# Kernel optimization log

Measured on AMD Instinct MI355X. Metric: run time of the kernel, lower is better.

The kernel has to match this reference:

```python
import jax, jax.numpy as jnp
import numpy as np

B, T, D, H = 1, 2048, 1024, 16
Dh = D // H
GSA_SCALE = 0.25
LN_EPS = 1e-5


def setup_inputs() -> dict:
    key = jax.random.key(0)
    ks = jax.random.split(key, 24)
    s = 0.02
    def W(k, din, dout):
        return jax.random.normal(k, (din, dout), jnp.float32) * s
    inp = dict(
        x=jax.random.normal(ks[0], (B, T, D), jnp.float32),
        mask=jnp.ones((B, T, T), jnp.bool_),
        # MultiHeadAttention params (linears[0..3] = q,k,v,o)
        mha_wq=W(ks[1], D, D), mha_bq=jnp.zeros((D,), jnp.float32),
        mha_wk=W(ks[2], D, D), mha_bk=jnp.zeros((D,), jnp.float32),
        mha_wv=W(ks[3], D, D), mha_bv=jnp.zeros((D,), jnp.float32),
        mha_wo=W(ks[4], D, D), mha_bo=jnp.zeros((D,), jnp.float32),
        # _GeodesicSelfAttention params
        gsa_wq=W(ks[5], D, D), gsa_bq=jnp.zeros((D,), jnp.float32),
        gsa_wk=W(ks[6], D, D), gsa_bk=jnp.zeros((D,), jnp.float32),
        gsa_wv=W(ks[7], D, D), gsa_bv=jnp.zeros((D,), jnp.float32),
        gsa_wo=W(ks[8], D, D), gsa_bo=jnp.zeros((D,), jnp.float32),
        log_diag=jnp.zeros((H, Dh), jnp.float32),  # nn.Parameter(torch.zeros(h, dk))
        # LayerNorms
        ln_mha_g=jnp.ones((D,), jnp.float32), ln_mha_b=jnp.zeros((D,), jnp.float32),
        ln_gsa_g=jnp.ones((D,), jnp.float32), ln_gsa_b=jnp.zeros((D,), jnp.float32),
        # mix scalar (initialized to -2.0 in __init__)
        gsa_mix=jnp.asarray(-2.0, jnp.float32),
        # gate: Linear(D,D) -> GELU -> Linear(D,1), last bias filled with 0.5
        gate_w1=W(ks[9], D, D), gate_b1=jnp.zeros((D,), jnp.float32),
        gate_w2=W(ks[10], D, 1), gate_b2=jnp.full((1,), 0.5, jnp.float32),
    )
    return inp


def _ln(x, g, b):
    m = x.mean(-1, keepdims=True)
    v = ((x - m) ** 2).mean(-1, keepdims=True)
    return (x - m) / jnp.sqrt(v + LN_EPS) * g + b


def _heads(y):  # [B,T,D] -> [B,H,T,Dh]
    return y.reshape(B, T, H, Dh).transpose(0, 2, 1, 3)


def _merge(y):  # [B,H,T,Dh] -> [B,T,D]
    return y.transpose(0, 2, 1, 3).reshape(B, T, D)


def _forward(x, mask, mha_wq, mha_bq, mha_wk, mha_bk, mha_wv, mha_bv, mha_wo, mha_bo,
             gsa_wq, gsa_bq, gsa_wk, gsa_bk, gsa_wv, gsa_bv, gsa_wo, gsa_bo,
             log_diag, ln_mha_g, ln_mha_b, ln_gsa_g, ln_gsa_b, gsa_mix,
             gate_w1, gate_b1, gate_w2, gate_b2):
    inv_sqrt_dh = 1.0 / jnp.sqrt(jnp.float32(Dh))
    m4 = mask[:, None, :, :]  # [B,1,T,T]

    # ---- standard MHA branch ----
    q = _heads(x @ mha_wq + mha_bq)
    k = _heads(x @ mha_wk + mha_bk)
    v = _heads(x @ mha_wv + mha_bv)
    scores = jnp.einsum('bhtd,bhsd->bhts', q, k) * inv_sqrt_dh
    scores = jnp.where(m4, scores, -jnp.inf)
    p = jax.nn.softmax(scores, axis=-1)
    mha_out = _merge(jnp.einsum('bhts,bhsd->bhtd', p, v)) @ mha_wo + mha_bo

    # ---- geodesic (Mahalanobis) branch ----
    qg = _heads(x @ gsa_wq + gsa_bq)
    kg = _heads(x @ gsa_wk + gsa_bk)
    vg = _heads(x @ gsa_wv + gsa_bv)
    diag = jax.nn.softplus(log_diag) + 1e-6          # [H,Dh]
    diag4 = diag[None, :, None, :]
    qM = qg * diag4
    q2M = (qg * qM).sum(-1)                           # [B,H,T]
    k2M = (kg * (kg * diag4)).sum(-1)                 # [B,H,T]
    cross = jnp.einsum('bhtd,bhsd->bhts', qM, kg)     # [B,H,T,T]
    dist = q2M[..., :, None] + k2M[..., None, :] - 2.0 * cross
    s = -0.5 * dist * inv_sqrt_dh
    s = jnp.where(m4, s, -jnp.inf)
    all_inf = jnp.all(jnp.isneginf(s), axis=-1, keepdims=True)
    s = jnp.where(all_inf, 0.0, s)
    pg = jax.nn.softmax(s * GSA_SCALE, axis=-1)
    gsa_out = _merge(jnp.einsum('bhts,bhsd->bhtd', pg, vg)) @ gsa_wo + gsa_bo

    # ---- gated mix ----
    mha_out = _ln(mha_out, ln_mha_g, ln_mha_b)
    gsa_out = jax.nn.sigmoid(gsa_mix) * _ln(gsa_out, ln_gsa_g, ln_gsa_b)
    g = jax.nn.gelu(x @ gate_w1 + gate_b1, approximate=False) @ gate_w2 + gate_b2
    alpha = 0.9 * jax.nn.sigmoid(g)                   # alpha_cap = 0.9, [B,T,1]
    return alpha * mha_out + (1.0 - alpha) * gsa_out


def reference(x, mask, mha_wq, mha_bq, mha_wk, mha_bk, mha_wv, mha_bv, mha_wo, mha_bo,
              gsa_wq, gsa_bq, gsa_wk, gsa_bk, gsa_wv, gsa_bv, gsa_wo, gsa_bo,
              log_diag, ln_mha_g, ln_mha_b, ln_gsa_g, ln_gsa_b, gsa_mix,
              gate_w1, gate_b1, gate_w2, gate_b2):
    return _forward(x, mask, mha_wq, mha_bq, mha_wk, mha_bk, mha_wv, mha_bv, mha_wo, mha_bo,
                    gsa_wq, gsa_bq, gsa_wk, gsa_bk, gsa_wv, gsa_bv, gsa_wo, gsa_bo,
                    log_diag, ln_mha_g, ln_mha_b, ln_gsa_g, ln_gsa_b, gsa_mix,
                    gate_w1, gate_b1, gate_w2, gate_b2)
```

## Files before the change

kernel.cpp:

```cpp
#include <hip/hip_runtime.h>
#include <stdint.h>

typedef unsigned short u16;
typedef u16   u16x4  __attribute__((ext_vector_type(4)));
typedef u16   u16x8  __attribute__((ext_vector_type(8)));
typedef __bf16 bf16x8 __attribute__((ext_vector_type(8)));
typedef float f32x4  __attribute__((ext_vector_type(4)));

#define SEQ   2048
#define DM    1024
#define NHEAD 16
#define DHEAD 64

#define QM_SCALE 0.180336880f
#define QG_SCALE 0.045084220f
#define K2_SCALE 0.022542110f

static __device__ __forceinline__ u16 f2b(float f) {
  uint32_t u = __float_as_uint(f);
  u += 0x7fffu + ((u >> 16) & 1u);
  return (u16)(u >> 16);
}
static __device__ __forceinline__ float b2f(u16 u) {
  return __uint_as_float(((uint32_t)u) << 16);
}

static __device__ __forceinline__ void gload16(const u16* g, u16* l) {
  __builtin_amdgcn_global_load_lds(
      (const __attribute__((address_space(1))) unsigned int*)g,
      (__attribute__((address_space(3))) unsigned int*)l, 16, 0, 0);
}

struct PrepArgs { const float* w[9]; u16* o[9];
                  const float* x; u16* xb; const float* log_diag; float* diag; };

__global__ __launch_bounds__(256) void prep_kernel(PrepArgs a) {
  const int z = blockIdx.z, tid = threadIdx.x;
  if (z == 9) {
    int b = blockIdx.y * 16 + blockIdx.x;
#pragma unroll
    for (int j = 0; j < 8; ++j) {
      int idx = b * 8192 + j * 1024 + tid * 4;
      float4 v = *(const float4*)&a.x[idx];
      u16x4 w = {f2b(v.x), f2b(v.y), f2b(v.z), f2b(v.w)};
      *(u16x4*)&a.xb[idx] = w;
    }
    if (b == 0) {
#pragma unroll
      for (int j = 0; j < 4; ++j) {
        int i = j * 256 + tid;
        float v = a.log_diag[i];
        float sp = (v > 20.f) ? v : log1pf(__expf(v));
        a.diag[i] = sp + 1e-6f;
      }
    }
    return;
  }
  const float* __restrict__ src = a.w[z];
  u16* __restrict__ dst = a.o[z];
  int r0 = blockIdx.y * 64, c0 = blockIdx.x * 64;
  __shared__ float tile[64][65];
  int r = tid >> 2, o8 = (tid & 3) * 16;
#pragma unroll
  for (int i = 0; i < 16; i += 4) {
    float4 v = *(const float4*)&src[(r0 + r) * DM + c0 + o8 + i];
    tile[r][o8 + i + 0] = v.x; tile[r][o8 + i + 1] = v.y;
    tile[r][o8 + i + 2] = v.z; tile[r][o8 + i + 3] = v.w;
  }
  __syncthreads();
  u16x8 w0, w1;
#pragma unroll
  for (int i = 0; i < 8; ++i) w0[i] = f2b(tile[o8 + i][r]);
#pragma unroll
  for (int i = 0; i < 8; ++i) w1[i] = f2b(tile[o8 + 8 + i][r]);
  *(u16x8*)&dst[(c0 + r) * DM + r0 + o8]     = w0;
  *(u16x8*)&dst[(c0 + r) * DM + r0 + o8 + 8] = w1;
}

struct GemmDesc { const u16* A; const u16* Bt; const float* bias; void* out;
                  float* aux; int mode; int k0; int klen; float scale; };
struct GemmParams { GemmDesc d[8]; const float* diag; };

__global__ __launch_bounds__(256) void gemm_bt_kernel(GemmParams p) {
  GemmDesc g = p.d[blockIdx.z];
  const int K = DM;
  const int m0 = blockIdx.y * 128, n0 = blockIdx.x * 64;
  const int tid = threadIdx.x;
  const int wave = tid >> 6, lane = tid & 63, ln = lane & 15, quad = lane >> 4;

  __shared__ __align__(16) u16 As[2 * 128 * 32];
  __shared__ __align__(16) u16 Bs[2 * 64 * 32];

  const f32x4 fz = {0.f, 0.f, 0.f, 0.f};
  f32x4 acc[2][4];
#pragma unroll
  for (int i = 0; i < 2; ++i)
#pragma unroll
    for (int j = 0; j < 4; ++j) acc[i][j] = fz;

  const u16* Aps[4]; const u16* Bps[2];
#pragma unroll
  for (int s = 0; s < 4; ++s) {
    int vr = s * 64 + (tid >> 2);
    Aps[s] = g.A + (size_t)(m0 + (vr & 127)) * K + g.k0 + (vr >> 7) * 32 + (tid & 3) * 8;
  }
#pragma unroll
  for (int s = 0; s < 2; ++s) {
    int vr = s * 64 + (tid >> 2);
    Bps[s] = g.Bt + (size_t)(n0 + (vr & 63)) * K + g.k0 + (vr >> 6) * 32 + (tid & 3) * 8;
  }

  for (int kk = 0; kk < g.klen; kk += 64) {
#pragma unroll
    for (int s = 0; s < 4; ++s) gload16(Aps[s] + kk, &As[s * 2048 + tid * 8]);
#pragma unroll
    for (int s = 0; s < 2; ++s) gload16(Bps[s] + kk, &Bs[s * 2048 + tid * 8]);
    __syncthreads();
#pragma unroll
    for (int c = 0; c < 2; ++c) {
      bf16x8 af[2], bfr[4];
#pragma unroll
      for (int mb = 0; mb < 2; ++mb)
        af[mb] = *(const bf16x8*)&As[(c * 128 + wave * 32 + mb * 16 + ln) * 32 + quad * 8];
#pragma unroll
      for (int nb = 0; nb < 4; ++nb)
        bfr[nb] = *(const bf16x8*)&Bs[(c * 64 + nb * 16 + ln) * 32 + quad * 8];
#pragma unroll
      for (int mb = 0; mb < 2; ++mb)
#pragma unroll
        for (int nb = 0; nb < 4; ++nb)
          acc[mb][nb] = __builtin_amdgcn_mfma_f32_16x16x32_bf16(af[mb], bfr[nb], acc[mb][nb], 0, 0, 0);
    }
    __syncthreads();
  }

  const int mode = g.mode;
  const int h = n0 >> 6;
#pragma unroll
  for (int mb = 0; mb < 2; ++mb) {
    int row = m0 + wave * 32 + mb * 16 + quad * 4;
    float ksum[4] = {0.f, 0.f, 0.f, 0.f};
#pragma unroll
    for (int nb = 0; nb < 4; ++nb) {
      int col = n0 + nb * 16 + ln;
      float bv = g.bias ? g.bias[col] : 0.f;
      f32x4 a = acc[mb][nb];
      if (mode == 5) {
        u16x4 w;
#pragma unroll
        for (int r = 0; r < 4; ++r) w[r] = f2b(a[r] + bv);
        *(u16x4*)&((u16*)g.out)[((size_t)(h * 64) + nb * 16 + ln) * SEQ + row] = w;
        continue;
      }
#pragma unroll
      for (int r = 0; r < 4; ++r) {
        float v = a[r] + bv;
        int rw = row + r;
        if (mode == 0) {
          ((u16*)g.out)[((size_t)h * SEQ + rw) * DHEAD + (col & 63)] = f2b(v);
        } else if (mode == 1) {
          ((u16*)g.out)[((size_t)h * SEQ + rw) * DHEAD + (col & 63)] = f2b(v * g.scale);
        } else if (mode == 2) {
          ((u16*)g.out)[((size_t)h * SEQ + rw) * DHEAD + (col & 63)] = f2b(v * p.diag[col] * g.scale);
        } else if (mode == 3) {
          float gg = 0.5f * v * (1.f + erff(v * 0.70710678f));
          ((u16*)g.out)[(size_t)rw * DM + col] = f2b(gg);
        } else if (mode == 4) {
          ((float*)g.out)[(size_t)rw * DM + col] = v;
        } else {
          ((u16*)g.out)[((size_t)h * SEQ + rw) * DHEAD + (col & 63)] = f2b(v);
          ksum[r] += v * v * p.diag[col];
        }
      }
    }
    if (mode == 6) {
#pragma unroll
      for (int r = 0; r < 4; ++r) {
        float s = ksum[r];
        s += __shfl_xor(s, 1); s += __shfl_xor(s, 2);
        s += __shfl_xor(s, 4); s += __shfl_xor(s, 8);
        if (ln == 0) g.aux[(size_t)h * SEQ + row + r] = s * K2_SCALE;
      }
    }
  }
}

__global__ __launch_bounds__(256) void flash_kernel(
    const u16* __restrict__ Qm, const u16* __restrict__ Km, const u16* __restrict__ VmT,
    const u16* __restrict__ Qg, const u16* __restrict__ Kg, const u16* __restrict__ VgT,
    const float* __restrict__ k2m, u16* __restrict__ attM, u16* __restrict__ attG) {
  const int z = blockIdx.z;
  const u16* __restrict__ Q  = z ? Qg  : Qm;
  const u16* __restrict__ Kp = z ? Kg  : Km;
  const u16* __restrict__ Vt = z ? VgT : VmT;
  u16* __restrict__ out = z ? attG : attM;
  const int h = blockIdx.y;
  const int tid = threadIdx.x, wave = tid >> 6, lane = tid & 63, ln = lane & 15, quad = lane >> 4;
  const int wrow = blockIdx.x * 128 + wave * 32;

  __shared__ __align__(16) u16 Ks[64 * 72];
  __shared__ __align__(16) u16 Vs[80 * 72];
  __shared__ __align__(16) u16 Pt[4][32 * 72];
  __shared__ float k2s[64];

  bf16x8 qf[2][2];
#pragma unroll
  for (int qb = 0; qb < 2; ++qb)
#pragma unroll
    for (int kb = 0; kb < 2; ++kb)
      qf[qb][kb] = *(const bf16x8*)&Q[((size_t)(h * SEQ) + wrow + qb * 16 + ln) * 64 + kb * 32 + quad * 8];

  const f32x4 fz = {0.f, 0.f, 0.f, 0.f};
  f32x4 o[2][5];
#pragma unroll
  for (int qb = 0; qb < 2; ++qb)
#pragma unroll
    for (int db = 0; db < 5; ++db) o[qb][db] = fz;

  const int sr = tid >> 2, sc = (tid & 3) * 16;
  const u16* Kbase = Kp + (size_t)h * SEQ * 64;
  const u16* Vbase = Vt + (size_t)h * 64 * SEQ;

  if (tid < 36) ((uint32_t*)&Vs[64 * 72])[tid] = 0x3F803F80u;

  u16x8 kr0 = *(const u16x8*)&Kbase[(size_t)sr * 64 + sc];
  u16x8 kr1 = *(const u16x8*)&Kbase[(size_t)sr * 64 + sc + 8];
  u16x8 vr0 = *(const u16x8*)&Vbase[(size_t)sr * SEQ + sc];
  u16x8 vr1 = *(const u16x8*)&Vbase[(size_t)sr * SEQ + sc + 8];
  float k2r = 0.f;
  if (z && tid < 64) k2r = k2m[h * SEQ + tid];

  for (int kt = 0; kt < SEQ; kt += 64) {
    *(u16x8*)&Ks[sr * 72 + sc]     = kr0;
    *(u16x8*)&Ks[sr * 72 + sc + 8] = kr1;
    *(u16x8*)&Vs[sr * 72 + sc]     = vr0;
    *(u16x8*)&Vs[sr * 72 + sc + 8] = vr1;
    if (z && tid < 64) k2s[tid] = k2r;
    __syncthreads();
    if (kt + 64 < SEQ) {
      kr0 = *(const u16x8*)&Kbase[(size_t)(kt + 64 + sr) * 64 + sc];
      kr1 = *(const u16x8*)&Kbase[(size_t)(kt + 64 + sr) * 64 + sc + 8];
      vr0 = *(const u16x8*)&Vbase[(size_t)sr * SEQ + kt + 64 + sc];
      vr1 = *(const u16x8*)&Vbase[(size_t)sr * SEQ + kt + 64 + sc + 8];
      if (z && tid < 64) k2r = k2m[h * SEQ + kt + 64 + tid];
    }

    bf16x8 kf0[4], kf1[4];
#pragma unroll
    for (int sb = 0; sb < 4; ++sb) {
      kf0[sb] = *(const bf16x8*)&Ks[(sb * 16 + ln) * 72 + quad * 8];
      kf1[sb] = *(const bf16x8*)&Ks[(sb * 16 + ln) * 72 + 32 + quad * 8];
    }

#pragma unroll
    for (int qb = 0; qb < 2; ++qb) {
      f32x4 st[4];
#pragma unroll
      for (int sb = 0; sb < 4; ++sb) {
        st[sb] = fz;
        st[sb] = __builtin_amdgcn_mfma_f32_16x16x32_bf16(kf0[sb], qf[qb][0], st[sb], 0, 0, 0);
        st[sb] = __builtin_amdgcn_mfma_f32_16x16x32_bf16(kf1[sb], qf[qb][1], st[sb], 0, 0, 0);
      }
#pragma unroll
      for (int sb = 0; sb < 4; ++sb) {
        if (z) {
          f32x4 b4 = *(const f32x4*)&k2s[sb * 16 + quad * 4];
#pragma unroll
          for (int r = 0; r < 4; ++r) st[sb][r] -= b4[r];
        }
        uint32_t eb[4];
#pragma unroll
        for (int r = 0; r < 4; ++r)
          eb[r] = __float_as_uint(__builtin_amdgcn_exp2f(st[sb][r]));
        uint32_t lo = __builtin_amdgcn_perm(eb[1], eb[0], 0x07060302u);
        uint32_t hi = __builtin_amdgcn_perm(eb[3], eb[2], 0x07060302u);
        uint2 pk = {lo, hi};
        *(uint2*)&Pt[wave][(qb * 16 + ln) * 72 + sb * 16 + quad * 4] = pk;
      }
    }
    __asm__ __volatile__("" ::: "memory");

    bf16x8 pf[2][2];
#pragma unroll
    for (int qb = 0; qb < 2; ++qb) {
      pf[qb][0] = *(const bf16x8*)&Pt[wave][(qb * 16 + ln) * 72 + quad * 8];
      pf[qb][1] = *(const bf16x8*)&Pt[wave][(qb * 16 + ln) * 72 + 32 + quad * 8];
    }
#pragma unroll
    for (int db = 0; db < 5; ++db) {
      bf16x8 vf0 = *(const bf16x8*)&Vs[(db * 16 + ln) * 72 + quad * 8];
      bf16x8 vf1 = *(const bf16x8*)&Vs[(db * 16 + ln) * 72 + 32 + quad * 8];
#pragma unroll
      for (int qb = 0; qb < 2; ++qb) {
        o[qb][db] = __builtin_amdgcn_mfma_f32_16x16x32_bf16(vf0, pf[qb][0], o[qb][db], 0, 0, 0);
        o[qb][db] = __builtin_amdgcn_mfma_f32_16x16x32_bf16(vf1, pf[qb][1], o[qb][db], 0, 0, 0);
      }
    }
    __syncthreads();
  }

#pragma unroll
  for (int qb = 0; qb < 2; ++qb) {
    float l_all = __shfl(o[qb][4][0], ln);
    float inv = 1.f / l_all;
#pragma unroll
    for (int db = 0; db < 4; ++db) {
      u16x4 w;
#pragma unroll
      for (int r = 0; r < 4; ++r) w[r] = f2b(o[qb][db][r] * inv);
      *(u16x4*)&out[(size_t)(wrow + qb * 16 + ln) * DM + h * 64 + db * 16 + quad * 4] = w;
    }
  }
}

__global__ __launch_bounds__(256) void final_kernel(
    const float* __restrict__ p0, const float* __restrict__ p1,
    const float* __restrict__ p2, const float* __restrict__ p3,
    const u16* __restrict__ G1, const float* __restrict__ w2,
    const float* __restrict__ b2, const float* __restrict__ mixp,
    const float* __restrict__ gm, const float* __restrict__ bm,
    const float* __restrict__ gg, const float* __restrict__ bg,
    float* __restrict__ out) {
  int t = blockIdx.x, tid = threadIdx.x;
  float xm[4], xg[4];
  float sm = 0.f, sm2 = 0.f, sg = 0.f, sg2 = 0.f, sd = 0.f;
#pragma unroll
  for (int j0 = 0; j0 < 4; ++j0) {
    int j = tid + j0 * 256;
    size_t idx = (size_t)t * DM + j;
    float a = p0[idx] + p1[idx];
    float b = p2[idx] + p3[idx];
    xm[j0] = a; xg[j0] = b;
    sm += a; sm2 += a * a; sg += b; sg2 += b * b;
    sd += b2f(G1[idx]) * w2[j];
  }
#pragma unroll
  for (int d = 32; d >= 1; d >>= 1) {
    sm += __shfl_xor(sm, d); sm2 += __shfl_xor(sm2, d);
    sg += __shfl_xor(sg, d); sg2 += __shfl_xor(sg2, d);
    sd += __shfl_xor(sd, d);
  }
  __shared__ float red[5][4];
  int wave = tid >> 6;
  if ((tid & 63) == 0) {
    red[0][wave] = sm; red[1][wave] = sm2; red[2][wave] = sg;
    red[3][wave] = sg2; red[4][wave] = sd;
  }
  __syncthreads();
  sm  = red[0][0] + red[0][1] + red[0][2] + red[0][3];
  sm2 = red[1][0] + red[1][1] + red[1][2] + red[1][3];
  sg  = red[2][0] + red[2][1] + red[2][2] + red[2][3];
  sg2 = red[3][0] + red[3][1] + red[3][2] + red[3][3];
  sd  = red[4][0] + red[4][1] + red[4][2] + red[4][3];

  float mm = sm / DM, vm = fmaxf(sm2 / DM - mm * mm, 0.f);
  float rm = rsqrtf(vm + 1e-5f);
  float mg = sg / DM, vg = fmaxf(sg2 / DM - mg * mg, 0.f);
  float rg = rsqrtf(vg + 1e-5f);
  float alpha = 0.9f / (1.f + __expf(-(sd + b2[0])));
  float mix = 1.f / (1.f + __expf(-mixp[0]));
#pragma unroll
  for (int j0 = 0; j0 < 4; ++j0) {
    int j = tid + j0 * 256;
    float lm = (xm[j0] - mm) * rm * gm[j] + bm[j];
    float lg = (xg[j0] - mg) * rg * gg[j] + bg[j];
    out[(size_t)t * DM + j] = alpha * lm + (1.f - alpha) * mix * lg;
  }
}

extern "C" void kernel_launch(void* const* d_in, const int* in_sizes, int n_in,
                              void* d_out, int out_size, void* d_ws, size_t ws_size,
                              hipStream_t stream) {
  const float* x        = (const float*)d_in[0];
  const float* mha_wq = (const float*)d_in[2];
  const float* mha_bq = (const float*)d_in[3];
  const float* mha_wk = (const float*)d_in[4];
  const float* mha_bk = (const float*)d_in[5];
  const float* mha_wv = (const float*)d_in[6];
  const float* mha_bv = (const float*)d_in[7];
  const float* mha_wo = (const float*)d_in[8];
  const float* mha_bo = (const float*)d_in[9];
  const float* gsa_wq = (const float*)d_in[10];
  const float* gsa_bq = (const float*)d_in[11];
  const float* gsa_wk = (const float*)d_in[12];
  const float* gsa_bk = (const float*)d_in[13];
  const float* gsa_wv = (const float*)d_in[14];
  const float* gsa_bv = (const float*)d_in[15];
  const float* gsa_wo = (const float*)d_in[16];
  const float* gsa_bo = (const float*)d_in[17];
  const float* log_diag = (const float*)d_in[18];
  const float* ln_mha_g = (const float*)d_in[19];
  const float* ln_mha_b = (const float*)d_in[20];
  const float* ln_gsa_g = (const float*)d_in[21];
  const float* ln_gsa_b = (const float*)d_in[22];
  const float* gsa_mix  = (const float*)d_in[23];
  const float* gate_w1  = (const float*)d_in[24];
  const float* gate_b1  = (const float*)d_in[25];
  const float* gate_w2  = (const float*)d_in[26];
  const float* gate_b2  = (const float*)d_in[27];

  char* ws = (char*)d_ws;
  size_t off = 0;
  auto alloc = [&](size_t bytes) -> void* {
    void* p = ws + off;
    off += (bytes + 255) & ~(size_t)255;
    return p;
  };

  u16* xb = (u16*)alloc((size_t)SEQ * DM * 2);
  u16* wT[9];
  for (int i = 0; i < 9; ++i) wT[i] = (u16*)alloc((size_t)DM * DM * 2);
  float* diag = (float*)alloc((size_t)DM * 4);
  u16* Qm  = (u16*)alloc((size_t)SEQ * DM * 2);
  u16* Km  = (u16*)alloc((size_t)SEQ * DM * 2);
  u16* Qg  = (u16*)alloc((size_t)SEQ * DM * 2);
  u16* Kg  = (u16*)alloc((size_t)SEQ * DM * 2);
  u16* VmT = (u16*)alloc((size_t)SEQ * DM * 2);
  u16* VgT = (u16*)alloc((size_t)SEQ * DM * 2);
  float* k2m = (float*)alloc((size_t)NHEAD * SEQ * 4);
  u16* G1   = (u16*)alloc((size_t)SEQ * DM * 2);
  u16* attM = (u16*)alloc((size_t)SEQ * DM * 2);
  u16* attG = (u16*)alloc((size_t)SEQ * DM * 2);
  float* proj3 = (float*)alloc((size_t)SEQ * DM * 4);
  float* proj0 = (float*)Qm;
  float* proj1 = (float*)Qg;
  float* proj2 = (float*)VmT;

  PrepArgs pa;
  pa.w[0] = mha_wq; pa.w[1] = mha_wk; pa.w[2] = mha_wv; pa.w[3] = mha_wo;
  pa.w[4] = gsa_wq; pa.w[5] = gsa_wk; pa.w[6] = gsa_wv; pa.w[7] = gsa_wo;
  pa.w[8] = gate_w1;
  for (int i = 0; i < 9; ++i) pa.o[i] = wT[i];
  pa.x = x; pa.xb = xb; pa.log_diag = log_diag; pa.diag = diag;
  prep_kernel<<<dim3(16, 16, 10), 256, 0, stream>>>(pa);

  GemmParams gp{};
  gp.diag = diag;
  gp.d[0] = {xb, wT[0], mha_bq, (void*)Qm,  nullptr, 1, 0, DM, QM_SCALE};
  gp.d[1] = {xb, wT[1], mha_bk, (void*)Km,  nullptr, 0, 0, DM, 1.f};
  gp.d[2] = {xb, wT[2], mha_bv, (void*)VmT, nullptr, 5, 0, DM, 1.f};
  gp.d[3] = {xb, wT[4], gsa_bq, (void*)Qg,  nullptr, 2, 0, DM, QG_SCALE};
  gp.d[4] = {xb, wT[5], gsa_bk, (void*)Kg,  k2m,     6, 0, DM, 1.f};
  gp.d[5] = {xb, wT[6], gsa_bv, (void*)VgT, nullptr, 5, 0, DM, 1.f};
  gp.d[6] = {xb, wT[8], gate_b1,(void*)G1,  nullptr, 3, 0, DM, 1.f};
  gemm_bt_kernel<<<dim3(16, 16, 7), 256, 0, stream>>>(gp);

  flash_kernel<<<dim3(SEQ / 128, NHEAD, 2), 256, 0, stream>>>(Qm, Km, VmT, Qg, Kg, VgT, k2m, attM, attG);

  GemmParams gp2{};
  gp2.diag = diag;
  gp2.d[0] = {attM, wT[3], mha_bo, (void*)proj0, nullptr, 4, 0,   512, 1.f};
  gp2.d[1] = {attM, wT[3], nullptr,(void*)proj1, nullptr, 4, 512, 512, 1.f};
  gp2.d[2] = {attG, wT[7], gsa_bo, (void*)proj2, nullptr, 4, 0,   512, 1.f};
  gp2.d[3] = {attG, wT[7], nullptr,(void*)proj3, nullptr, 4, 512, 512, 1.f};
  gemm_bt_kernel<<<dim3(16, 16, 4), 256, 0, stream>>>(gp2);

  final_kernel<<<SEQ, 256, 0, stream>>>(proj0, proj1, proj2, proj3, G1,
                                        gate_w2, gate_b2, gsa_mix,
                                        ln_mha_g, ln_mha_b, ln_gsa_g, ln_gsa_b,
                                        (float*)d_out);
}
```

Before: 290.3 us.

## Enlarge GEMM tiles to 256x256 with double-buffered swizzled LDS

```diff
diff --git a/kernel.cpp b/kernel.cpp
--- a/kernel.cpp
+++ b/kernel.cpp
@@ -81,75 +81,88 @@
                   float* aux; int mode; int k0; int klen; float scale; };
 struct GemmParams { GemmDesc d[8]; const float* diag; };
 
-__global__ __launch_bounds__(256) void gemm_bt_kernel(GemmParams p) {
+__global__ __launch_bounds__(512) void gemm_bt_kernel(GemmParams p) {
   GemmDesc g = p.d[blockIdx.z];
   const int K = DM;
-  const int m0 = blockIdx.y * 128, n0 = blockIdx.x * 64;
+  const int m0 = blockIdx.y * 256, n0 = blockIdx.x * 256;
   const int tid = threadIdx.x;
   const int wave = tid >> 6, lane = tid & 63, ln = lane & 15, quad = lane >> 4;
-
-  __shared__ __align__(16) u16 As[2 * 128 * 32];
-  __shared__ __align__(16) u16 Bs[2 * 64 * 32];
+  const int wm = wave >> 2, wn = wave & 3;
+
+  __shared__ __align__(16) u16 As[2][256 * 64];
+  __shared__ __align__(16) u16 Bs[2][256 * 64];
 
   const f32x4 fz = {0.f, 0.f, 0.f, 0.f};
-  f32x4 acc[2][4];
-#pragma unroll
-  for (int i = 0; i < 2; ++i)
+  f32x4 acc[8][4];
+#pragma unroll
+  for (int i = 0; i < 8; ++i)
 #pragma unroll
     for (int j = 0; j < 4; ++j) acc[i][j] = fz;
 
-  const u16* Aps[4]; const u16* Bps[2];
-#pragma unroll
-  for (int s = 0; s < 4; ++s) {
-    int vr = s * 64 + (tid >> 2);
-    Aps[s] = g.A + (size_t)(m0 + (vr & 127)) * K + g.k0 + (vr >> 7) * 32 + (tid & 3) * 8;
-  }
-#pragma unroll
-  for (int s = 0; s < 2; ++s) {
-    int vr = s * 64 + (tid >> 2);
-    Bps[s] = g.Bt + (size_t)(n0 + (vr & 63)) * K + g.k0 + (vr >> 6) * 32 + (tid & 3) * 8;
-  }
-
-  for (int kk = 0; kk < g.klen; kk += 64) {
-#pragma unroll
-    for (int s = 0; s < 4; ++s) gload16(Aps[s] + kk, &As[s * 2048 + tid * 8]);
-#pragma unroll
-    for (int s = 0; s < 2; ++s) gload16(Bps[s] + kk, &Bs[s * 2048 + tid * 8]);
+  const int trow  = tid >> 3;
+  const int dslot = (tid & 7) ^ (trow & 7);
+  const u16* Ap = g.A  + (size_t)(m0 + trow) * K + g.k0 + dslot * 8;
+  const u16* Bp = g.Bt + (size_t)(n0 + trow) * K + g.k0 + dslot * 8;
+
+#pragma unroll
+  for (int s = 0; s < 4; ++s)
+    gload16(Ap + (size_t)s * 64 * K, &As[0][s * 4096 + tid * 8]);
+#pragma unroll
+  for (int s = 0; s < 4; ++s)
+    gload16(Bp + (size_t)s * 64 * K, &Bs[0][s * 4096 + tid * 8]);
+  __syncthreads();
+
+  const int nt = g.klen >> 6;
+  int cur = 0;
+  for (int t = 0; t < nt; ++t) {
+    if (t + 1 < nt) {
+      const int kk = (t + 1) << 6;
+#pragma unroll
+      for (int s = 0; s < 4; ++s)
+        gload16(Ap + (size_t)s * 64 * K + kk, &As[cur ^ 1][s * 4096 + tid * 8]);
+#pragma unroll
+      for (int s = 0; s < 4; ++s)
+        gload16(Bp + (size_t)s * 64 * K + kk, &Bs[cur ^ 1][s * 4096 + tid * 8]);
+    }
+
+    bf16x8 bfr[4][2];
+#pragma unroll
+    for (int nb = 0; nb < 4; ++nb) {
+      const int br = wn * 64 + nb * 16 + ln;
+#pragma unroll
+      for (int kh = 0; kh < 2; ++kh)
+        bfr[nb][kh] = *(const bf16x8*)&Bs[cur][br * 64 + (((kh << 2) + quad) ^ (br & 7)) * 8];
+    }
+#pragma unroll
+    for (int mb = 0; mb < 8; ++mb) {
+      const int ar = wm * 128 + mb * 16 + ln;
+      bf16x8 af0 = *(const bf16x8*)&As[cur][ar * 64 + ((quad)     ^ (ar & 7)) * 8];
+      bf16x8 af1 = *(const bf16x8*)&As[cur][ar * 64 + ((4 + quad) ^ (ar & 7)) * 8];
+#pragma unroll
+      for (int nb = 0; nb < 4; ++nb) {
+        acc[mb][nb] = __builtin_amdgcn_mfma_f32_16x16x32_bf16(af0, bfr[nb][0], acc[mb][nb], 0, 0, 0);
+        acc[mb][nb] = __builtin_amdgcn_mfma_f32_16x16x32_bf16(af1, bfr[nb][1], acc[mb][nb], 0, 0, 0);
+      }
+    }
     __syncthreads();
-#pragma unroll
-    for (int c = 0; c < 2; ++c) {
-      bf16x8 af[2], bfr[4];
-#pragma unroll
-      for (int mb = 0; mb < 2; ++mb)
-        af[mb] = *(const bf16x8*)&As[(c * 128 + wave * 32 + mb * 16 + ln) * 32 + quad * 8];
-#pragma unroll
-      for (int nb = 0; nb < 4; ++nb)
-        bfr[nb] = *(const bf16x8*)&Bs[(c * 64 + nb * 16 + ln) * 32 + quad * 8];
-#pragma unroll
-      for (int mb = 0; mb < 2; ++mb)
-#pragma unroll
-        for (int nb = 0; nb < 4; ++nb)
-          acc[mb][nb] = __builtin_amdgcn_mfma_f32_16x16x32_bf16(af[mb], bfr[nb], acc[mb][nb], 0, 0, 0);
-    }
-    __syncthreads();
+    cur ^= 1;
   }
 
   const int mode = g.mode;
-  const int h = n0 >> 6;
-#pragma unroll
-  for (int mb = 0; mb < 2; ++mb) {
-    int row = m0 + wave * 32 + mb * 16 + quad * 4;
+#pragma unroll
+  for (int mb = 0; mb < 8; ++mb) {
+    int row = m0 + wm * 128 + mb * 16 + quad * 4;
     float ksum[4] = {0.f, 0.f, 0.f, 0.f};
 #pragma unroll
     for (int nb = 0; nb < 4; ++nb) {
-      int col = n0 + nb * 16 + ln;
+      int col = n0 + wn * 64 + nb * 16 + ln;
       float bv = g.bias ? g.bias[col] : 0.f;
       f32x4 a = acc[mb][nb];
       if (mode == 5) {
         u16x4 w;
 #pragma unroll
         for (int r = 0; r < 4; ++r) w[r] = f2b(a[r] + bv);
-        *(u16x4*)&((u16*)g.out)[((size_t)(h * 64) + nb * 16 + ln) * SEQ + row] = w;
+        *(u16x4*)&((u16*)g.out)[(size_t)col * SEQ + row] = w;
         continue;
       }
 #pragma unroll
@@ -157,23 +170,24 @@
         float v = a[r] + bv;
         int rw = row + r;
         if (mode == 0) {
-          ((u16*)g.out)[((size_t)h * SEQ + rw) * DHEAD + (col & 63)] = f2b(v);
+          ((u16*)g.out)[((size_t)(col >> 6) * SEQ + rw) * DHEAD + (col & 63)] = f2b(v);
         } else if (mode == 1) {
-          ((u16*)g.out)[((size_t)h * SEQ + rw) * DHEAD + (col & 63)] = f2b(v * g.scale);
+          ((u16*)g.out)[((size_t)(col >> 6) * SEQ + rw) * DHEAD + (col & 63)] = f2b(v * g.scale);
         } else if (mode == 2) {
-          ((u16*)g.out)[((size_t)h * SEQ + rw) * DHEAD + (col & 63)] = f2b(v * p.diag[col] * g.scale);
+          ((u16*)g.out)[((size_t)(col >> 6) * SEQ + rw) * DHEAD + (col & 63)] = f2b(v * p.diag[col] * g.scale);
         } else if (mode == 3) {
           float gg = 0.5f * v * (1.f + erff(v * 0.70710678f));
           ((u16*)g.out)[(size_t)rw * DM + col] = f2b(gg);
         } else if (mode == 4) {
           ((float*)g.out)[(size_t)rw * DM + col] = v;
         } else {
-          ((u16*)g.out)[((size_t)h * SEQ + rw) * DHEAD + (col & 63)] = f2b(v);
+          ((u16*)g.out)[((size_t)(col >> 6) * SEQ + rw) * DHEAD + (col & 63)] = f2b(v);
           ksum[r] += v * v * p.diag[col];
         }
       }
     }
     if (mode == 6) {
+      const int h = (n0 >> 6) + wn;
 #pragma unroll
       for (int r = 0; r < 4; ++r) {
         float s = ksum[r];
@@ -443,7 +457,7 @@
   gp.d[4] = {xb, wT[5], gsa_bk, (void*)Kg,  k2m,     6, 0, DM, 1.f};
   gp.d[5] = {xb, wT[6], gsa_bv, (void*)VgT, nullptr, 5, 0, DM, 1.f};
   gp.d[6] = {xb, wT[8], gate_b1,(void*)G1,  nullptr, 3, 0, DM, 1.f};
-  gemm_bt_kernel<<<dim3(16, 16, 7), 256, 0, stream>>>(gp);
+  gemm_bt_kernel<<<dim3(4, 8, 7), 512, 0, stream>>>(gp);
 
   flash_kernel<<<dim3(SEQ / 128, NHEAD, 2), 256, 0, stream>>>(Qm, Km, VmT, Qg, Kg, VgT, k2m, attM, attG);
 
@@ -453,7 +467,7 @@
   gp2.d[1] = {attM, wT[3], nullptr,(void*)proj1, nullptr, 4, 512, 512, 1.f};
   gp2.d[2] = {attG, wT[7], gsa_bo, (void*)proj2, nullptr, 4, 0,   512, 1.f};
   gp2.d[3] = {attG, wT[7], nullptr,(void*)proj3, nullptr, 4, 512, 512, 1.f};
-  gemm_bt_kernel<<<dim3(16, 16, 4), 256, 0, stream>>>(gp2);
+  gemm_bt_kernel<<<dim3(4, 8, 4), 512, 0, stream>>>(gp2);
 
   final_kernel<<<SEQ, 256, 0, stream>>>(proj0, proj1, proj2, proj3, G1,
                                         gate_w2, gate_b2, gsa_mix,
```

After: 511.5 us. +76.2%, slower.
